# Kernel optimization log

Measured on AMD Instinct MI355X. Metric: run time of the kernel, lower is better.

Reference implementation:

```python
import jax, jax.numpy as jnp
import numpy as np
from jax import lax


def conv2d(x, w, padding):
    # x: [B,C,H,W], w: [O,I,kh,kw]; torch Conv2d == cross-correlation, same as lax default
    return lax.conv_general_dilated(x, w, (1, 1), padding,
                                    dimension_numbers=('NCHW', 'OIHW', 'NCHW'))


def setup_inputs() -> dict:
    key = jax.random.key(0)
    ks = jax.random.split(key, 16)
    B, C1, C2, H1, W1, H2, W2, ratio = 8, 256, 512, 64, 64, 32, 32, 8
    Cr = C1 // ratio  # 32
    s = 0.05
    return {
        'x1': jax.random.normal(ks[0], (B, C1, H1, W1), jnp.float32),
        'x2': jax.random.normal(ks[1], (B, C2, H2, W2), jnp.float32),
        'wq': jax.random.normal(ks[2], (Cr, C1, 3, 3), jnp.float32) * s,
        'wk': jax.random.normal(ks[3], (Cr, C2, 3, 3), jnp.float32) * s,
        'wv': jax.random.normal(ks[4], (C1, C2, 3, 3), jnp.float32) * s,
        'wc': jax.random.normal(ks[5], (1, C1, 1, 1), jnp.float32) * s,
        'wch': jax.random.normal(ks[6], (C1, C1, 3, 3), jnp.float32) * s,
        'wt1': jax.random.normal(ks[7], (Cr, C1, 1, 1), jnp.float32) * s,
        'bt1': jax.random.normal(ks[8], (Cr,), jnp.float32) * s,
        'ln_g': jnp.ones((Cr, 1, 1), jnp.float32),
        'ln_b': jnp.zeros((Cr, 1, 1), jnp.float32),
        'wt2': jax.random.normal(ks[9], (C1, Cr, 1, 1), jnp.float32) * s,
        'bt2': jax.random.normal(ks[10], (C1,), jnp.float32) * s,
    }


def reference(x1, x2, wq, wk, wv, wc, wch, wt1, bt1, ln_g, ln_b, wt2, bt2):
    B, C1, H1, W1 = x1.shape
    N1 = H1 * W1
    N2 = x2.shape[2] * x2.shape[3]
    eps = 1e-5

    # spatial cross-attention branch
    q = conv2d(x1, wq, 'SAME').reshape(B, -1, N1)          # [B,Cr,N1]
    k = conv2d(x2, wk, 'SAME').reshape(B, -1, N2)          # [B,Cr,N2]
    v = conv2d(x2, wv, 'SAME').reshape(B, C1, N2)          # [B,C1,N2]
    content = jnp.einsum('bcn,bcm->bnm', k, q)             # [B,N2,N1] (key^T @ query)
    content = jax.nn.softmax(content, axis=1)              # softmax over N2 (dim=1)
    att_con = jnp.einsum('bcn,bnm->bcm', v, content).reshape(B, C1, H1, W1) + x1

    # channel attention branch
    cf = conv2d(x1, wc, 'VALID').reshape(B, 1, N1)         # 1x1 conv -> [B,1,N1]
    cf = jax.nn.softmax(cf.transpose(0, 2, 1), axis=1)     # [B,N1,1], softmax over N1
    chf = conv2d(x1, wch, 'SAME').reshape(B, C1, N1)       # [B,C1,N1]
    pool = jnp.einsum('bcn,bno->bco', chf, cf).reshape(B, C1, 1, 1)

    t = conv2d(pool, wt1, 'VALID') + bt1.reshape(1, -1, 1, 1)  # [B,Cr,1,1]
    mu = jnp.mean(t, axis=(1, 2, 3), keepdims=True)
    var = jnp.mean((t - mu) ** 2, axis=(1, 2, 3), keepdims=True)
    t = (t - mu) * lax.rsqrt(var + eps) * ln_g[None] + ln_b[None]
    t = jax.nn.relu(t)
    channel_weight = conv2d(t, wt2, 'VALID') + bt2.reshape(1, -1, 1, 1)  # [B,C1,1,1]

    return att_con + x1 * channel_weight
```

## Files before the change

### kernel.cpp

```cpp
#include <hip/hip_runtime.h>
#include <stdint.h>

#define LL long long

typedef short short8 __attribute__((ext_vector_type(8)));
typedef short short4v __attribute__((ext_vector_type(4)));
typedef float f32x4 __attribute__((ext_vector_type(4)));
typedef unsigned int uint2v __attribute__((ext_vector_type(2)));

__device__ __forceinline__ unsigned short f2bf(float f) {
  unsigned u = __float_as_uint(f);
  unsigned r = (u + 0x7fffu + ((u >> 16) & 1u)) >> 16;
  return (unsigned short)r;
}
__device__ __forceinline__ float bf2f(unsigned short h) {
  return __uint_as_float(((unsigned)h) << 16);
}

#define MFMA16(A, B, C) __builtin_amdgcn_mfma_f32_16x16x32_bf16(A, B, C, 0, 0, 0)

__global__ __launch_bounds__(256) void wtrans2(
    const float* __restrict__ src, unsigned short* __restrict__ dh,
    unsigned short* __restrict__ dl, int OC, int IC)
{
  const int i = blockIdx.x * 256 + threadIdx.x;
  if (i >= OC * IC * 9) return;
  const int off = i % 9;
  const int rest = i / 9;
  const int ic = rest % IC;
  const int oc = rest / IC;
  const float v = src[i];
  const unsigned short h = f2bf(v);
  const LL di = (((LL)off * (IC >> 5) + (ic >> 5)) * OC + oc) * 32 + (ic & 31);
  dh[di] = h;
  if (dl) dl[di] = f2bf(v - bf2f(h));
}

__global__ __launch_bounds__(256) void transp(
    const float* __restrict__ src, unsigned short* __restrict__ dh,
    unsigned short* __restrict__ dl, int C, int N)
{
  __shared__ unsigned short sh[64 * 66];
  __shared__ unsigned short sl[64 * 66];
  const int t = threadIdx.x;
  const int b = blockIdx.z;
  const int n0 = blockIdx.x * 64, c0 = blockIdx.y * 64;
  {
    const int nl = t & 63, cl0 = t >> 6;
#pragma unroll
    for (int i = 0; i < 16; ++i) {
      const int cl = cl0 + 4 * i;
      const float v = src[((LL)b * C + c0 + cl) * N + n0 + nl];
      const unsigned short h = f2bf(v);
      sh[nl * 66 + cl] = h;
      sl[nl * 66 + cl] = f2bf(v - bf2f(h));
    }
  }
  __syncthreads();
  {
    const int cl = t & 63, nr0 = t >> 6;
    const int chunk = (c0 + cl) >> 5;
    const int cin = cl & 31;
#pragma unroll
    for (int j = 0; j < 16; ++j) {
      const int nr = nr0 + 4 * j;
      const LL di = (((LL)b * (C >> 5) + chunk) * N + n0 + nr) * 32 + cin;
      dh[di] = sh[nr * 66 + cl];
      if (dl) dl[di] = sl[nr * 66 + cl];
    }
  }
}

__global__ __launch_bounds__(256) void conv_qk_r(
    const unsigned short* __restrict__ xh, const unsigned short* __restrict__ xl,
    const unsigned short* __restrict__ wh, const unsigned short* __restrict__ wl,
    float* __restrict__ outp, int logW, int H, int C, int chunks_per)
{
  const int t = threadIdx.x, w = t >> 6, lane = t & 63;
  const int lo4 = lane & 15, hi4 = lane >> 4;
  const int b = blockIdx.z;
  const int W = 1 << logW;
  const int N = H * W;
  const int px0 = (blockIdx.x * 4 + w) * 32;
  const int row = px0 >> logW;
  const int x0 = px0 & (W - 1);
  const int nch = C >> 5;
  const int ch0 = blockIdx.y * chunks_per;
  const short8 zero8 = {0, 0, 0, 0, 0, 0, 0, 0};

  f32x4 acc[2][2];
#pragma unroll
  for (int p = 0; p < 2; ++p)
#pragma unroll
    for (int ot = 0; ot < 2; ++ot) acc[p][ot] = (f32x4){0.f, 0.f, 0.f, 0.f};

  for (int ch = ch0; ch < ch0 + chunks_per; ++ch) {
    const LL xbase = ((LL)(b * nch + ch)) * N * 32 + hi4 * 8;
#pragma unroll
    for (int ky = 0; ky < 3; ++ky) {
      const int gy = row + ky - 1;
      const bool oky = (unsigned)gy < (unsigned)H;
      const int gyc = min(max(gy, 0), H - 1);
#pragma unroll
      for (int kx = 0; kx < 3; ++kx) {
        short8 Bh[2], Bl[2];
#pragma unroll
        for (int p = 0; p < 2; ++p) {
          const int gx = x0 + p * 16 + lo4 + kx - 1;
          const bool ok = oky && ((unsigned)gx < (unsigned)W);
          const int gxc = min(max(gx, 0), W - 1);
          const LL xoff = xbase + (LL)(gyc * W + gxc) * 32;
          const short8 bh = *(const short8*)(xh + xoff);
          const short8 bl = *(const short8*)(xl + xoff);
          Bh[p] = ok ? bh : zero8;
          Bl[p] = ok ? bl : zero8;
        }
        const int off = ky * 3 + kx;
        short8 Ah[2], Al[2];
#pragma unroll
        for (int ot = 0; ot < 2; ++ot) {
          const LL wi = ((LL)(off * nch + ch) * 32 + ot * 16 + lo4) * 32 + hi4 * 8;
          Ah[ot] = *(const short8*)(wh + wi);
          Al[ot] = *(const short8*)(wl + wi);
        }
#pragma unroll
        for (int p = 0; p < 2; ++p)
#pragma unroll
          for (int ot = 0; ot < 2; ++ot) {
            acc[p][ot] = MFMA16(Ah[ot], Bh[p], acc[p][ot]);
            acc[p][ot] = MFMA16(Ah[ot], Bl[p], acc[p][ot]);
            acc[p][ot] = MFMA16(Al[ot], Bh[p], acc[p][ot]);
          }
      }
    }
  }
  float* op = outp + (LL)blockIdx.y * 8 * N * 32;
#pragma unroll
  for (int p = 0; p < 2; ++p)
#pragma unroll
    for (int ot = 0; ot < 2; ++ot) {
      const LL o = ((LL)b * N + px0 + p * 16 + lo4) * 32 + ot * 16 + hi4 * 4;
      *(f32x4*)(op + o) = acc[p][ot];
    }
}

__global__ __launch_bounds__(256) void red_split(
    const float* __restrict__ src, unsigned short* __restrict__ dh,
    unsigned short* __restrict__ dl, int nparts, int n4)
{
  const int i = blockIdx.x * 256 + threadIdx.x;
  if (i >= n4) return;
  f32x4 a = ((const f32x4*)src)[i];
  for (int p = 1; p < nparts; ++p)
    a += ((const f32x4*)src)[(LL)p * n4 + i];
  short4v hv, lv;
#pragma unroll
  for (int j = 0; j < 4; ++j) {
    const unsigned short h = f2bf(a[j]);
    hv[j] = (short)h;
    lv[j] = (short)f2bf(a[j] - bf2f(h));
  }
  ((short4v*)dh)[i] = hv;
  ((short4v*)dl)[i] = lv;
}

__global__ __launch_bounds__(512) void conv_v_r(
    const unsigned short* __restrict__ xh, const unsigned short* __restrict__ wt,
    unsigned short* __restrict__ out)
{
  __shared__ float sred[16][4][64];
  const int t = threadIdx.x, w = t >> 6, lane = t & 63;
  const int lo4 = lane & 15, hi4 = lane >> 4;
  const int b = blockIdx.z;
  const int kh = w >> 2, wsub = w & 3;
  const int row = blockIdx.x * 2 + (wsub & 1);
  const int ocb = blockIdx.y * 64 + (wsub >> 1) * 32;
  const short8 zero8 = {0, 0, 0, 0, 0, 0, 0, 0};

  f32x4 acc[2][2];
#pragma unroll
  for (int p = 0; p < 2; ++p)
#pragma unroll
    for (int o = 0; o < 2; ++o) acc[p][o] = (f32x4){0.f, 0.f, 0.f, 0.f};

  for (int ch = kh * 8; ch < kh * 8 + 8; ++ch) {
    const LL xchb = ((LL)(b * 16 + ch)) * 1024 * 32 + hi4 * 8;
#pragma unroll
    for (int ky = 0; ky < 3; ++ky) {
      const int gy = row + ky - 1;
      const bool oky = (unsigned)gy < 32u;
      const int gyc = min(max(gy, 0), 31);
      short8 Bt[3][2], At[3][2];
#pragma unroll
      for (int kx = 0; kx < 3; ++kx) {
#pragma unroll
        for (int p = 0; p < 2; ++p) {
          const int gx = p * 16 + lo4 + kx - 1;
          const bool ok = oky && ((unsigned)gx < 32u);
          const int gxc = min(max(gx, 0), 31);
          const short8 bv = *(const short8*)(xh + xchb + (LL)(gyc * 32 + gxc) * 32);
          Bt[kx][p] = ok ? bv : zero8;
        }
        const int off = ky * 3 + kx;
#pragma unroll
        for (int o = 0; o < 2; ++o)
          At[kx][o] = *(const short8*)(
              wt + ((LL)(off * 16 + ch) * 256 + ocb + o * 16 + lo4) * 32 + hi4 * 8);
      }
#pragma unroll
      for (int kx = 0; kx < 3; ++kx)
#pragma unroll
        for (int p = 0; p < 2; ++p)
#pragma unroll
          for (int o = 0; o < 2; ++o)
            acc[p][o] = MFMA16(At[kx][o], Bt[kx][p], acc[p][o]);
    }
  }
  if (w >= 4) {
#pragma unroll
    for (int p = 0; p < 2; ++p)
#pragma unroll
      for (int o = 0; o < 2; ++o)
#pragma unroll
        for (int r = 0; r < 4; ++r)
          sred[p * 8 + o * 4 + r][wsub][lane] = acc[p][o][r];
  }
  __syncthreads();
  if (w < 4) {
#pragma unroll
    for (int p = 0; p < 2; ++p)
#pragma unroll
      for (int o = 0; o < 2; ++o)
#pragma unroll
        for (int r = 0; r < 4; ++r) {
          const float v = acc[p][o][r] + sred[p * 8 + o * 4 + r][wsub][lane];
          const int oc = ocb + o * 16 + hi4 * 4 + r;
          out[(((LL)b * 32 + row) * 256 + oc) * 32 + p * 16 + lo4] = f2bf(v);
        }
  }
}

__global__ __launch_bounds__(256) void cf_dot(
    const float* __restrict__ x1, const float* __restrict__ wc, float* __restrict__ cf)
{
  const int b = blockIdx.y;
  const int n = blockIdx.x * 256 + threadIdx.x;
  const float* xp = x1 + (LL)b * 256 * 4096 + n;
  float a = 0.f;
#pragma unroll 4
  for (int c = 0; c < 256; ++c)
    a = fmaf(xp[(LL)c * 4096], wc[c], a);
  cf[b * 4096 + n] = a;
}

__global__ __launch_bounds__(1024) void cf_softmax(
    const float* __restrict__ cf, float* __restrict__ cfs)
{
  const int b = blockIdx.x, t = threadIdx.x;
  __shared__ float r1[16];
  __shared__ float r2[16];
  float v[4];
#pragma unroll
  for (int j = 0; j < 4; ++j) v[j] = cf[b * 4096 + t + 1024 * j];
  float mx = fmaxf(fmaxf(v[0], v[1]), fmaxf(v[2], v[3]));
#pragma unroll
  for (int k = 1; k <= 32; k <<= 1) mx = fmaxf(mx, __shfl_xor(mx, k));
  const int wv = t >> 6;
  if ((t & 63) == 0) r1[wv] = mx;
  __syncthreads();
  float m2 = r1[0];
#pragma unroll
  for (int i = 1; i < 16; ++i) m2 = fmaxf(m2, r1[i]);
  float e[4]; float s = 0.f;
#pragma unroll
  for (int j = 0; j < 4; ++j) { e[j] = __expf(v[j] - m2); s += e[j]; }
#pragma unroll
  for (int k = 1; k <= 32; k <<= 1) s += __shfl_xor(s, k);
  if ((t & 63) == 0) r2[wv] = s;
  __syncthreads();
  float s2 = 0.f;
#pragma unroll
  for (int i = 0; i < 16; ++i) s2 += r2[i];
  const float inv = 1.f / s2;
#pragma unroll
  for (int j = 0; j < 4; ++j) cfs[b * 4096 + t + 1024 * j] = e[j] * inv;
}

__global__ __launch_bounds__(256) void ykern(
    const float* __restrict__ x1, const float* __restrict__ cfs, float* __restrict__ T)
{
  __shared__ float cl[6][64];
  const int chunk = blockIdx.x, b = blockIdx.y, t = threadIdx.x;
  for (int idx = t; idx < 384; idx += 256) {
    int lr = idx >> 6, col = idx & 63;
    int gr = chunk * 4 - 1 + lr;
    cl[lr][col] = ((unsigned)gr < 64u) ? cfs[b * 4096 + gr * 64 + col] : 0.f;
  }
  __syncthreads();
  const int c = t;
  float a[9];
#pragma unroll
  for (int k = 0; k < 9; ++k) a[k] = 0.f;
  const float* xp = x1 + ((LL)b * 256 + c) * 4096 + chunk * 256;
  for (int i = 0; i < 256; ++i) {
    float xv = xp[i];
    int yl = i >> 6, col = i & 63;
#pragma unroll
    for (int dy = 0; dy < 3; ++dy) {
      int lr = yl + 2 - dy;
#pragma unroll
      for (int dx = 0; dx < 3; ++dx) {
        int cc = col + 1 - dx;
        float f = ((unsigned)cc < 64u) ? cl[lr][cc] : 0.f;
        a[dy * 3 + dx] = fmaf(xv, f, a[dy * 3 + dx]);
      }
    }
  }
#pragma unroll
  for (int k = 0; k < 9; ++k)
    atomicAdd(&T[((LL)b * 256 + c) * 9 + k], a[k]);
}

__global__ __launch_bounds__(256) void pool_k(
    const float* __restrict__ T, const float* __restrict__ wch,
    float* __restrict__ pool)
{
  __shared__ __align__(16) float Tl[2304];
  const int b = blockIdx.y, ocg = blockIdx.x;
  const int t = threadIdx.x, w = t >> 6, lane = t & 63;
  for (int i = t; i < 2304; i += 256) Tl[i] = T[(LL)b * 2304 + i];
  __syncthreads();
  const float4* tp = (const float4*)Tl;
#pragma unroll
  for (int oi = 0; oi < 2; ++oi) {
    const int oc = ocg * 8 + w * 2 + oi;
    const float4* wp = (const float4*)(wch + (LL)oc * 2304);
    float a = 0.f;
#pragma unroll
    for (int j = 0; j < 9; ++j) {
      const int idx = lane + 64 * j;
      float4 w4 = wp[idx], t4 = tp[idx];
      a = fmaf(w4.x, t4.x, a); a = fmaf(w4.y, t4.y, a);
      a = fmaf(w4.z, t4.z, a); a = fmaf(w4.w, t4.w, a);
    }
#pragma unroll
    for (int k = 1; k <= 32; k <<= 1) a += __shfl_xor(a, k);
    if (lane == 0) pool[b * 256 + oc] = a;
  }
}

__global__ __launch_bounds__(256) void chw_tail(
    const float* __restrict__ pool_g,
    const float* __restrict__ wt1, const float* __restrict__ bt1,
    const float* __restrict__ lng, const float* __restrict__ lnb,
    const float* __restrict__ wt2, const float* __restrict__ bt2,
    float* __restrict__ cwp1)
{
  const int b = blockIdx.x, t = threadIdx.x;
  __shared__ float pool[256];
  __shared__ float tt[32];
  pool[t] = pool_g[b * 256 + t];
  __syncthreads();
  if (t < 64) {
    float tv = 0.f;
    if (t < 32) {
      const float* wp = wt1 + (LL)t * 256;
      for (int c = 0; c < 256; ++c) tv = fmaf(wp[c], pool[c], tv);
      tv += bt1[t];
    }
    float s = tv;
#pragma unroll
    for (int k = 1; k <= 16; k <<= 1) s += __shfl_xor(s, k);
    float mu = s * (1.f / 32.f);
    float d = tv - mu;
    float vs = d * d;
#pragma unroll
    for (int k = 1; k <= 16; k <<= 1) vs += __shfl_xor(vs, k);
    float var = vs * (1.f / 32.f);
    if (t < 32) {
      float nrm = d / sqrtf(var + 1e-5f);
      float y = nrm * lng[t] + lnb[t];
      tt[t] = fmaxf(y, 0.f);
    }
  }
  __syncthreads();
  {
    float s2 = bt2[t];
    const float* wp = wt2 + (LL)t * 32;
#pragma unroll
    for (int i = 0; i < 32; ++i) s2 = fmaf(wp[i], tt[i], s2);
    cwp1[b * 256 + t] = 1.f + s2;
  }
}

__global__ __launch_bounds__(256) void attn_stats(
    const unsigned short* __restrict__ qh_g, const unsigned short* __restrict__ ql_g,
    const unsigned short* __restrict__ kh_g, const unsigned short* __restrict__ kl_g,
    float* __restrict__ mxs, float* __restrict__ invl)
{
  const int t = threadIdx.x, w = t >> 6, lane = t & 63;
  const int lo4 = lane & 15, hi4 = lane >> 4;
  const int b = blockIdx.y, mc = blockIdx.x * 64;
  const float L2E = 1.4426950408889634f;

  short8 qh[4], ql[4];
#pragma unroll
  for (int mt = 0; mt < 4; ++mt) {
    const LL qa = ((LL)(b * 4096 + mc + mt * 16 + lo4)) * 32 + hi4 * 8;
    qh[mt] = *(const short8*)(qh_g + qa);
    ql[mt] = *(const short8*)(ql_g + qa);
  }

  float M[4], L[4];
#pragma unroll
  for (int mt = 0; mt < 4; ++mt) { M[mt] = -1e30f; L[mt] = 0.f; }

  for (int ns = 0; ns < 16; ++ns) {
    const int n = w * 256 + ns * 16 + lo4;
    const LL ka = ((LL)(b * 1024 + n)) * 32 + hi4 * 8;
    const short8 kh = *(const short8*)(kh_g + ka);
    const short8 kl = *(const short8*)(kl_g + ka);
#pragma unroll
    for (int mt = 0; mt < 4; ++mt) {
      f32x4 s = {0.f, 0.f, 0.f, 0.f};
      s = MFMA16(kl, qh[mt], s);
      s = MFMA16(kh, ql[mt], s);
      s = MFMA16(kh, qh[mt], s);
      float lm = fmaxf(fmaxf(s[0], s[1]), fmaxf(s[2], s[3]));
      float nM = fmaxf(M[mt], lm);
      float sc = exp2f((M[mt] - nM) * L2E);
      L[mt] = L[mt] * sc + exp2f((s[0] - nM) * L2E) + exp2f((s[1] - nM) * L2E)
                         + exp2f((s[2] - nM) * L2E) + exp2f((s[3] - nM) * L2E);
      M[mt] = nM;
    }
  }
#pragma unroll
  for (int mask = 16; mask <= 32; mask <<= 1) {
#pragma unroll
    for (int mt = 0; mt < 4; ++mt) {
      float oM = __shfl_xor(M[mt], mask), oL = __shfl_xor(L[mt], mask);
      float nM = fmaxf(M[mt], oM);
      L[mt] = L[mt] * exp2f((M[mt] - nM) * L2E) + oL * exp2f((oM - nM) * L2E);
      M[mt] = nM;
    }
  }
  __shared__ float sM[4][64], sL[4][64];
  if (lane < 16) {
#pragma unroll
    for (int mt = 0; mt < 4; ++mt) {
      sM[w][mt * 16 + lane] = M[mt];
      sL[w][mt * 16 + lane] = L[mt];
    }
  }
  __syncthreads();
  if (t < 64) {
    float Mg = sM[0][t], Lg = sL[0][t];
#pragma unroll
    for (int wv = 1; wv < 4; ++wv) {
      float oM = sM[wv][t], oL = sL[wv][t];
      float nM = fmaxf(Mg, oM);
      Lg = Lg * exp2f((Mg - nM) * L2E) + oL * exp2f((oM - nM) * L2E);
      Mg = nM;
    }
    mxs[b * 4096 + mc + t] = Mg * L2E;
    invl[b * 4096 + mc + t] = 1.f / Lg;
  }
}

__global__ __launch_bounds__(256) void attn_pv(
    const unsigned short* __restrict__ qh_g, const unsigned short* __restrict__ ql_g,
    const unsigned short* __restrict__ kh_g, const unsigned short* __restrict__ kl_g,
    const unsigned short* __restrict__ v16,
    const float* __restrict__ mxs, const float* __restrict__ invl,
    const float* __restrict__ x1, const float* __restrict__ cwp1,
    float* __restrict__ out)
{
  __shared__ __align__(16) unsigned short Pt[2][32][136];
  const int t = threadIdx.x, w = t >> 6, lane = t & 63;
  const int lo4 = lane & 15, hi4 = lane >> 4;
  const int b = blockIdx.y, mb = blockIdx.x * 32;
  const float L2E = 1.4426950408889634f;

  short8 qh[2], ql[2];
  float mxv[2], ilv[2];
#pragma unroll
  for (int mt = 0; mt < 2; ++mt) {
    const int m = mb + mt * 16 + lo4;
    const LL qa = ((LL)(b * 4096 + m)) * 32 + hi4 * 8;
    qh[mt] = *(const short8*)(qh_g + qa);
    ql[mt] = *(const short8*)(ql_g + qa);
    mxv[mt] = mxs[b * 4096 + m];
    ilv[mt] = invl[b * 4096 + m];
  }

  f32x4 acc[4][2];
#pragma unroll
  for (int ct = 0; ct < 4; ++ct)
#pragma unroll
    for (int mt = 0; mt < 2; ++mt) acc[ct][mt] = (f32x4){0.f, 0.f, 0.f, 0.f};

  short8 kh[2], kl[2];
#pragma unroll
  for (int ns = 0; ns < 2; ++ns) {
    const LL ka = ((LL)(b * 1024 + w * 32 + ns * 16 + lo4)) * 32 + hi4 * 8;
    kh[ns] = *(const short8*)(kh_g + ka);
    kl[ns] = *(const short8*)(kl_g + ka);
  }

  int buf = 0;
  for (int nt = 0; nt < 8; ++nt) {
    short8 knh[2], knl[2];
    {
      const int ntn = (nt + 1) & 7;
#pragma unroll
      for (int ns = 0; ns < 2; ++ns) {
        const LL ka = ((LL)(b * 1024 + ntn * 128 + w * 32 + ns * 16 + lo4)) * 32 + hi4 * 8;
        knh[ns] = *(const short8*)(kh_g + ka);
        knl[ns] = *(const short8*)(kl_g + ka);
      }
    }
    f32x4 s[2][2];
#pragma unroll
    for (int ns = 0; ns < 2; ++ns)
#pragma unroll
      for (int mt = 0; mt < 2; ++mt) {
        f32x4 z = {0.f, 0.f, 0.f, 0.f};
        z = MFMA16(kl[ns], qh[mt], z);
        z = MFMA16(kh[ns], ql[mt], z);
        z = MFMA16(kh[ns], qh[mt], z);
        s[ns][mt] = z;
      }
    short8 vpre[2][4];
#pragma unroll
    for (int ks = 0; ks < 2; ++ks)
#pragma unroll
      for (int ct = 0; ct < 4; ++ct)
        vpre[ks][ct] = *(const short8*)(
            v16 + (((LL)b * 32 + nt * 4 + ks) * 256 + w * 64 + ct * 16 + lo4) * 32 + hi4 * 8);
#pragma unroll
    for (int ns = 0; ns < 2; ++ns)
#pragma unroll
      for (int mt = 0; mt < 2; ++mt) {
        const int m_loc = mt * 16 + lo4;
        const int nl = w * 32 + ns * 16 + hi4 * 4;
        float p0 = exp2f(fmaf(s[ns][mt][0], L2E, -mxv[mt])) * ilv[mt];
        float p1 = exp2f(fmaf(s[ns][mt][1], L2E, -mxv[mt])) * ilv[mt];
        float p2 = exp2f(fmaf(s[ns][mt][2], L2E, -mxv[mt])) * ilv[mt];
        float p3 = exp2f(fmaf(s[ns][mt][3], L2E, -mxv[mt])) * ilv[mt];
        uint2v u;
        u[0] = (unsigned)f2bf(p0) | ((unsigned)f2bf(p1) << 16);
        u[1] = (unsigned)f2bf(p2) | ((unsigned)f2bf(p3) << 16);
        *(uint2v*)&Pt[buf][m_loc][nl] = u;
      }
    __syncthreads();
#pragma unroll
    for (int ks = 0; ks < 4; ++ks) {
      short8 pb[2];
#pragma unroll
      for (int mt = 0; mt < 2; ++mt)
        pb[mt] = *(const short8*)&Pt[buf][mt * 16 + lo4][ks * 32 + hi4 * 8];
#pragma unroll
      for (int ct = 0; ct < 4; ++ct) {
        const short8 va = (ks < 2)
            ? vpre[ks][ct]
            : *(const short8*)(
                  v16 + (((LL)b * 32 + nt * 4 + ks) * 256 + w * 64 + ct * 16 + lo4) * 32 + hi4 * 8);
#pragma unroll
        for (int mt = 0; mt < 2; ++mt)
          acc[ct][mt] = MFMA16(va, pb[mt], acc[ct][mt]);
      }
    }
    buf ^= 1;
#pragma unroll
    for (int ns = 0; ns < 2; ++ns) { kh[ns] = knh[ns]; kl[ns] = knl[ns]; }
  }

#pragma unroll
  for (int ct = 0; ct < 4; ++ct)
#pragma unroll
    for (int mt = 0; mt < 2; ++mt) {
      const int m = mb + mt * 16 + lo4;
#pragma unroll
      for (int r = 0; r < 4; ++r) {
        const int c = w * 64 + ct * 16 + hi4 * 4 + r;
        const float cw = cwp1[b * 256 + c];
        const LL off = ((LL)(b * 256 + c)) * 4096 + m;
        out[off] = acc[ct][mt][r] + x1[off] * cw;
      }
    }
}

extern "C" void kernel_launch(void* const* d_in, const int* in_sizes, int n_in,
                              void* d_out, int out_size, void* d_ws, size_t ws_size,
                              hipStream_t stream) {
  const float* x1  = (const float*)d_in[0];
  const float* x2  = (const float*)d_in[1];
  const float* wq  = (const float*)d_in[2];
  const float* wk  = (const float*)d_in[3];
  const float* wv  = (const float*)d_in[4];
  const float* wc  = (const float*)d_in[5];
  const float* wch = (const float*)d_in[6];
  const float* wt1 = (const float*)d_in[7];
  const float* bt1 = (const float*)d_in[8];
  const float* lng = (const float*)d_in[9];
  const float* lnb = (const float*)d_in[10];
  const float* wt2 = (const float*)d_in[11];
  const float* bt2 = (const float*)d_in[12];
  float* outp = (float*)d_out;

  float* ws   = (float*)d_ws;
  float* qtf  = ws;
  float* ktf  = qtf + 1048576;
  float* mxsb = ktf + 262144;
  float* invb = mxsb + 32768;
  float* cfr  = invb + 32768;
  float* cfs  = cfr + 32768;
  float* Tb   = cfs + 32768;
  float* cwb  = Tb + 18432;
  unsigned short* sbase = (unsigned short*)(cwb + 2048);
  unsigned short* v16  = sbase;
  unsigned short* x1th = v16  + 2097152;
  unsigned short* x1tl = x1th + 8388608;
  unsigned short* x2th = x1tl + 8388608;
  unsigned short* x2tl = x2th + 4194304;
  unsigned short* wvt  = x2tl + 4194304;
  unsigned short* wqh  = wvt  + 1179648;
  unsigned short* wql  = wqh  + 73728;
  unsigned short* wkh  = wql  + 73728;
  unsigned short* wkl  = wkh  + 147456;

  unsigned short* qhg = (unsigned short*)qtf;
  unsigned short* qlg = qhg + 1048576;
  unsigned short* khg = (unsigned short*)ktf;
  unsigned short* klg = khg + 262144;

  float* ktp = qtf;
  float* qtp = (float*)x2th;

  hipMemsetAsync(Tb, 0, (size_t)18432 * 4, stream);

  wtrans2<<<dim3(4608), 256, 0, stream>>>(wv, wvt, nullptr, 256, 512);
  wtrans2<<<dim3(288),  256, 0, stream>>>(wq, wqh, wql, 32, 256);
  wtrans2<<<dim3(576),  256, 0, stream>>>(wk, wkh, wkl, 32, 512);

  transp<<<dim3(64, 4, 8), 256, 0, stream>>>(x1, x1th, x1tl, 256, 4096);
  transp<<<dim3(16, 8, 8), 256, 0, stream>>>(x2, x2th, x2tl, 512, 1024);

  conv_qk_r<<<dim3(8, 4, 8), 256, 0, stream>>>(x2th, x2tl, wkh, wkl, ktp, 5, 32, 512, 4);
  red_split<<<dim3(256), 256, 0, stream>>>(ktp, khg, klg, 4, 65536);

  conv_v_r<<<dim3(16, 4, 8), 512, 0, stream>>>(x2th, wvt, v16);

  conv_qk_r<<<dim3(32, 4, 8), 256, 0, stream>>>(x1th, x1tl, wqh, wql, qtp, 6, 64, 256, 2);
  red_split<<<dim3(1024), 256, 0, stream>>>(qtp, qhg, qlg, 4, 262144);

  cf_dot<<<dim3(16, 8), 256, 0, stream>>>(x1, wc, cfr);
  cf_softmax<<<dim3(8), 1024, 0, stream>>>(cfr, cfs);
  ykern<<<dim3(16, 8), 256, 0, stream>>>(x1, cfs, Tb);
  pool_k<<<dim3(32, 8), 256, 0, stream>>>(Tb, wch, cfr);
  chw_tail<<<dim3(8), 256, 0, stream>>>(cfr, wt1, bt1, lng, lnb, wt2, bt2, cwb);

  attn_stats<<<dim3(64, 8), 256, 0, stream>>>(qhg, qlg, khg, klg, mxsb, invb);
  attn_pv<<<dim3(128, 8), 256, 0, stream>>>(qhg, qlg, khg, klg, v16, mxsb, invb, x1, cwb, outp);
}
```

Before: 447.9 us.

## Move conv split-K reduction into shared memory and drop red_split kernels

The q/k convolutions now assign each input-channel chunk to a separate wave within one block. Partial sums are reduced through shared memory and written straight out as bf16 hi/lo, which removes the fp32 partial-buffer round trip and the two red_split launches. The v convolution is reorganised so that 8 waves split the channels four ways over two row tiles with a smaller output-channel tile, and the reduction is spread across all waves. The trade-off is larger blocks (1024 threads) with big shared-memory footprints, which may reduce occupancy, and per-element scattered bf16 stores.

```diff
diff --git a/kernel.cpp b/kernel.cpp
--- a/kernel.cpp
+++ b/kernel.cpp
@@ -4,7 +4,6 @@
 #define LL long long
 
 typedef short short8 __attribute__((ext_vector_type(8)));
-typedef short short4v __attribute__((ext_vector_type(4)));
 typedef float f32x4 __attribute__((ext_vector_type(4)));
 typedef unsigned int uint2v __attribute__((ext_vector_type(2)));
 
@@ -71,21 +70,23 @@
   }
 }
 
-__global__ __launch_bounds__(256) void conv_qk_r(
+template<int NW>
+__global__ __launch_bounds__(NW * 64) void conv_qk_s(
     const unsigned short* __restrict__ xh, const unsigned short* __restrict__ xl,
     const unsigned short* __restrict__ wh, const unsigned short* __restrict__ wl,
-    float* __restrict__ outp, int logW, int H, int C, int chunks_per)
-{
+    unsigned short* __restrict__ dh, unsigned short* __restrict__ dl,
+    int logW, int H)
+{
+  __shared__ float sred[NW][16][64];
   const int t = threadIdx.x, w = t >> 6, lane = t & 63;
   const int lo4 = lane & 15, hi4 = lane >> 4;
   const int b = blockIdx.z;
   const int W = 1 << logW;
   const int N = H * W;
-  const int px0 = (blockIdx.x * 4 + w) * 32;
+  const int px0 = blockIdx.x * 32;
   const int row = px0 >> logW;
   const int x0 = px0 & (W - 1);
-  const int nch = C >> 5;
-  const int ch0 = blockIdx.y * chunks_per;
+  const int ch = w;
   const short8 zero8 = {0, 0, 0, 0, 0, 0, 0, 0};
 
   f32x4 acc[2][2];
@@ -94,87 +95,78 @@
 #pragma unroll
     for (int ot = 0; ot < 2; ++ot) acc[p][ot] = (f32x4){0.f, 0.f, 0.f, 0.f};
 
-  for (int ch = ch0; ch < ch0 + chunks_per; ++ch) {
-    const LL xbase = ((LL)(b * nch + ch)) * N * 32 + hi4 * 8;
-#pragma unroll
-    for (int ky = 0; ky < 3; ++ky) {
-      const int gy = row + ky - 1;
-      const bool oky = (unsigned)gy < (unsigned)H;
-      const int gyc = min(max(gy, 0), H - 1);
-#pragma unroll
-      for (int kx = 0; kx < 3; ++kx) {
-        short8 Bh[2], Bl[2];
-#pragma unroll
-        for (int p = 0; p < 2; ++p) {
-          const int gx = x0 + p * 16 + lo4 + kx - 1;
-          const bool ok = oky && ((unsigned)gx < (unsigned)W);
-          const int gxc = min(max(gx, 0), W - 1);
-          const LL xoff = xbase + (LL)(gyc * W + gxc) * 32;
-          const short8 bh = *(const short8*)(xh + xoff);
-          const short8 bl = *(const short8*)(xl + xoff);
-          Bh[p] = ok ? bh : zero8;
-          Bl[p] = ok ? bl : zero8;
+  const LL xbase = ((LL)(b * NW + ch)) * N * 32 + hi4 * 8;
+#pragma unroll
+  for (int ky = 0; ky < 3; ++ky) {
+    const int gy = row + ky - 1;
+    const bool oky = (unsigned)gy < (unsigned)H;
+    const int gyc = min(max(gy, 0), H - 1);
+#pragma unroll
+    for (int kx = 0; kx < 3; ++kx) {
+      short8 Bh[2], Bl[2];
+#pragma unroll
+      for (int p = 0; p < 2; ++p) {
+        const int gx = x0 + p * 16 + lo4 + kx - 1;
+        const bool ok = oky && ((unsigned)gx < (unsigned)W);
+        const int gxc = min(max(gx, 0), W - 1);
+        const LL xoff = xbase + (LL)(gyc * W + gxc) * 32;
+        const short8 bh = *(const short8*)(xh + xoff);
+        const short8 bl = *(const short8*)(xl + xoff);
+        Bh[p] = ok ? bh : zero8;
+        Bl[p] = ok ? bl : zero8;
+      }
+      const int off = ky * 3 + kx;
+      short8 Ah[2], Al[2];
+#pragma unroll
+      for (int ot = 0; ot < 2; ++ot) {
+        const LL wi = ((LL)(off * NW + ch) * 32 + ot * 16 + lo4) * 32 + hi4 * 8;
+        Ah[ot] = *(const short8*)(wh + wi);
+        Al[ot] = *(const short8*)(wl + wi);
+      }
+#pragma unroll
+      for (int p = 0; p < 2; ++p)
+#pragma unroll
+        for (int ot = 0; ot < 2; ++ot) {
+          acc[p][ot] = MFMA16(Ah[ot], Bh[p], acc[p][ot]);
+          acc[p][ot] = MFMA16(Ah[ot], Bl[p], acc[p][ot]);
+          acc[p][ot] = MFMA16(Al[ot], Bh[p], acc[p][ot]);
         }
-        const int off = ky * 3 + kx;
-        short8 Ah[2], Al[2];
-#pragma unroll
-        for (int ot = 0; ot < 2; ++ot) {
-          const LL wi = ((LL)(off * nch + ch) * 32 + ot * 16 + lo4) * 32 + hi4 * 8;
-          Ah[ot] = *(const short8*)(wh + wi);
-          Al[ot] = *(const short8*)(wl + wi);
-        }
-#pragma unroll
-        for (int p = 0; p < 2; ++p)
-#pragma unroll
-          for (int ot = 0; ot < 2; ++ot) {
-            acc[p][ot] = MFMA16(Ah[ot], Bh[p], acc[p][ot]);
-            acc[p][ot] = MFMA16(Ah[ot], Bl[p], acc[p][ot]);
-            acc[p][ot] = MFMA16(Al[ot], Bh[p], acc[p][ot]);
-          }
-      }
-    }
-  }
-  float* op = outp + (LL)blockIdx.y * 8 * N * 32;
+    }
+  }
 #pragma unroll
   for (int p = 0; p < 2; ++p)
 #pragma unroll
-    for (int ot = 0; ot < 2; ++ot) {
-      const LL o = ((LL)b * N + px0 + p * 16 + lo4) * 32 + ot * 16 + hi4 * 4;
-      *(f32x4*)(op + o) = acc[p][ot];
-    }
-}
-
-__global__ __launch_bounds__(256) void red_split(
-    const float* __restrict__ src, unsigned short* __restrict__ dh,
-    unsigned short* __restrict__ dl, int nparts, int n4)
-{
-  const int i = blockIdx.x * 256 + threadIdx.x;
-  if (i >= n4) return;
-  f32x4 a = ((const f32x4*)src)[i];
-  for (int p = 1; p < nparts; ++p)
-    a += ((const f32x4*)src)[(LL)p * n4 + i];
-  short4v hv, lv;
-#pragma unroll
-  for (int j = 0; j < 4; ++j) {
-    const unsigned short h = f2bf(a[j]);
-    hv[j] = (short)h;
-    lv[j] = (short)f2bf(a[j] - bf2f(h));
-  }
-  ((short4v*)dh)[i] = hv;
-  ((short4v*)dl)[i] = lv;
-}
-
-__global__ __launch_bounds__(512) void conv_v_r(
+    for (int ot = 0; ot < 2; ++ot)
+#pragma unroll
+      for (int r = 0; r < 4; ++r)
+        sred[w][p * 8 + ot * 4 + r][lane] = acc[p][ot][r];
+  __syncthreads();
+  constexpr int SPW = 16 / NW;
+#pragma unroll
+  for (int si = 0; si < SPW; ++si) {
+    const int slot = w * SPW + si;
+    float v = sred[0][slot][lane];
+#pragma unroll
+    for (int j = 1; j < NW; ++j) v += sred[j][slot][lane];
+    const int p = slot >> 3, ot = (slot >> 2) & 1, r = slot & 3;
+    const LL di = ((LL)b * N + px0 + p * 16 + lo4) * 32 + ot * 16 + hi4 * 4 + r;
+    const unsigned short h = f2bf(v);
+    dh[di] = h;
+    dl[di] = f2bf(v - bf2f(h));
+  }
+}
+
+__global__ __launch_bounds__(512) void conv_v_s(
     const unsigned short* __restrict__ xh, const unsigned short* __restrict__ wt,
     unsigned short* __restrict__ out)
 {
-  __shared__ float sred[16][4][64];
+  __shared__ float sred[8][16][64];
   const int t = threadIdx.x, w = t >> 6, lane = t & 63;
   const int lo4 = lane & 15, hi4 = lane >> 4;
   const int b = blockIdx.z;
-  const int kh = w >> 2, wsub = w & 3;
-  const int row = blockIdx.x * 2 + (wsub & 1);
-  const int ocb = blockIdx.y * 64 + (wsub >> 1) * 32;
+  const int tile = w & 1, kp = w >> 1;
+  const int row = blockIdx.x * 2 + tile;
+  const int ocb = blockIdx.y * 32;
   const short8 zero8 = {0, 0, 0, 0, 0, 0, 0, 0};
 
   f32x4 acc[2][2];
@@ -183,60 +175,56 @@
 #pragma unroll
     for (int o = 0; o < 2; ++o) acc[p][o] = (f32x4){0.f, 0.f, 0.f, 0.f};
 
-  for (int ch = kh * 8; ch < kh * 8 + 8; ++ch) {
+  for (int ch = kp * 4; ch < kp * 4 + 4; ++ch) {
     const LL xchb = ((LL)(b * 16 + ch)) * 1024 * 32 + hi4 * 8;
 #pragma unroll
     for (int ky = 0; ky < 3; ++ky) {
       const int gy = row + ky - 1;
       const bool oky = (unsigned)gy < 32u;
       const int gyc = min(max(gy, 0), 31);
-      short8 Bt[3][2], At[3][2];
 #pragma unroll
       for (int kx = 0; kx < 3; ++kx) {
+        short8 Bf[2];
 #pragma unroll
         for (int p = 0; p < 2; ++p) {
           const int gx = p * 16 + lo4 + kx - 1;
           const bool ok = oky && ((unsigned)gx < 32u);
           const int gxc = min(max(gx, 0), 31);
           const short8 bv = *(const short8*)(xh + xchb + (LL)(gyc * 32 + gxc) * 32);
-          Bt[kx][p] = ok ? bv : zero8;
+          Bf[p] = ok ? bv : zero8;
         }
         const int off = ky * 3 + kx;
+        short8 Af[2];
 #pragma unroll
         for (int o = 0; o < 2; ++o)
-          At[kx][o] = *(const short8*)(
+          Af[o] = *(const short8*)(
               wt + ((LL)(off * 16 + ch) * 256 + ocb + o * 16 + lo4) * 32 + hi4 * 8);
-      }
-#pragma unroll
-      for (int kx = 0; kx < 3; ++kx)
 #pragma unroll
         for (int p = 0; p < 2; ++p)
 #pragma unroll
           for (int o = 0; o < 2; ++o)
-            acc[p][o] = MFMA16(At[kx][o], Bt[kx][p], acc[p][o]);
-    }
-  }
-  if (w >= 4) {
-#pragma unroll
-    for (int p = 0; p < 2; ++p)
-#pragma unroll
-      for (int o = 0; o < 2; ++o)
-#pragma unroll
-        for (int r = 0; r < 4; ++r)
-          sred[p * 8 + o * 4 + r][wsub][lane] = acc[p][o][r];
-  }
-  __syncthreads();
-  if (w < 4) {
-#pragma unroll
-    for (int p = 0; p < 2; ++p)
-#pragma unroll
-      for (int o = 0; o < 2; ++o)
-#pragma unroll
-        for (int r = 0; r < 4; ++r) {
-          const float v = acc[p][o][r] + sred[p * 8 + o * 4 + r][wsub][lane];
-          const int oc = ocb + o * 16 + hi4 * 4 + r;
-          out[(((LL)b * 32 + row) * 256 + oc) * 32 + p * 16 + lo4] = f2bf(v);
-        }
+            acc[p][o] = MFMA16(Af[o], Bf[p], acc[p][o]);
+      }
+    }
+  }
+#pragma unroll
+  for (int p = 0; p < 2; ++p)
+#pragma unroll
+    for (int o = 0; o < 2; ++o)
+#pragma unroll
+      for (int r = 0; r < 4; ++r)
+        sred[w][p * 8 + o * 4 + r][lane] = acc[p][o][r];
+  __syncthreads();
+  const int tw = w & 1;
+  const int rowt = blockIdx.x * 2 + tw;
+#pragma unroll
+  for (int si = 0; si < 4; ++si) {
+    const int slot = (w >> 1) * 4 + si;
+    const float v = sred[tw][slot][lane] + sred[2 + tw][slot][lane]
+                  + sred[4 + tw][slot][lane] + sred[6 + tw][slot][lane];
+    const int p = slot >> 3, o = (slot >> 2) & 1, r = slot & 3;
+    const int oc = ocb + o * 16 + hi4 * 4 + r;
+    out[(((LL)b * 32 + rowt) * 256 + oc) * 32 + p * 16 + lo4] = f2bf(v);
   }
 }
 
@@ -634,9 +622,6 @@
   unsigned short* khg = (unsigned short*)ktf;
   unsigned short* klg = khg + 262144;
 
-  float* ktp = qtf;
-  float* qtp = (float*)x2th;
-
   hipMemsetAsync(Tb, 0, (size_t)18432 * 4, stream);
 
   wtrans2<<<dim3(4608), 256, 0, stream>>>(wv, wvt, nullptr, 256, 512);
@@ -646,13 +631,13 @@
   transp<<<dim3(64, 4, 8), 256, 0, stream>>>(x1, x1th, x1tl, 256, 4096);
   transp<<<dim3(16, 8, 8), 256, 0, stream>>>(x2, x2th, x2tl, 512, 1024);
 
-  conv_qk_r<<<dim3(8, 4, 8), 256, 0, stream>>>(x2th, x2tl, wkh, wkl, ktp, 5, 32, 512, 4);
-  red_split<<<dim3(256), 256, 0, stream>>>(ktp, khg, klg, 4, 65536);
-
-  conv_v_r<<<dim3(16, 4, 8), 512, 0, stream>>>(x2th, wvt, v16);
-
-  conv_qk_r<<<dim3(32, 4, 8), 256, 0, stream>>>(x1th, x1tl, wqh, wql, qtp, 6, 64, 256, 2);
-  red_split<<<dim3(1024), 256, 0, stream>>>(qtp, qhg, qlg, 4, 262144);
+  conv_qk_s<16><<<dim3(32, 1, 8), 1024, 0, stream>>>(
+      x2th, x2tl, wkh, wkl, khg, klg, 5, 32);
+
+  conv_v_s<<<dim3(16, 8, 8), 512, 0, stream>>>(x2th, wvt, v16);
+
+  conv_qk_s<8><<<dim3(128, 1, 8), 512, 0, stream>>>(
+      x1th, x1tl, wqh, wql, qhg, qlg, 6, 64);
 
   cf_dot<<<dim3(16, 8), 256, 0, stream>>>(x1, wc, cfr);
   cf_softmax<<<dim3(8), 1024, 0, stream>>>(cfr, cfs);
```

Result: faster. 427.7 us (-4.5%).
